# Performance work log

Measured on AMD Instinct MI355X. Metric: run time of the kernel, lower is better.

## Reference

```python
import jax, jax.numpy as jnp
import numpy as np

# module hyperparameters (match init_kwargs)
IN_PLANES = 64
OUT = 64            # out_planes
N_HASHES = 4
CHUNK = 25          # chunk_size
GROUPS = 8
KS = 56             # kernel_size == attended axis length H
GP = OUT // GROUPS  # group_planes = 8
EPS_N = 5e-5        # F.normalize eps
BN_EPS = 1e-5
F_GW, F_GV1, F_GV2 = 0.1, 0.1, 1.0


def l2norm(x, axis):
    # torch F.normalize(p=2, eps=EPS_N)
    n = jnp.sqrt(jnp.sum(x * x, axis=axis, keepdims=True))
    return x / jnp.maximum(n, EPS_N)


def setup_inputs() -> dict:
    key = jax.random.key(0)
    k1, k2, k3, k4 = jax.random.split(key, 4)
    x = jax.random.normal(k1, (2, IN_PLANES, KS, 56), jnp.float32)
    conv_w = jax.random.normal(k2, (OUT * 3 // 2, IN_PLANES), jnp.float32) * np.float32(np.sqrt(1.0 / IN_PLANES))
    bn_gamma = jnp.ones((OUT * 3 // 2,), jnp.float32)
    bn_beta = jnp.zeros((OUT * 3 // 2,), jnp.float32)
    relative = jax.random.normal(k3, (KS, GP * 3 // 2), jnp.float32) * np.float32(np.sqrt(1.0 / GP))
    # LSH random rotations: hash_buckets = min(56//25 + (56//25)%2, 10) = 2 -> hb//2 = 1
    rotations = jax.random.normal(k4, (OUT // 2, N_HASHES, 1), jnp.float32)
    return dict(x=x, conv_w=conv_w, bn_gamma=bn_gamma, bn_beta=bn_beta,
                relative=relative, rotations=rotations)


def reference(x, conv_w, bn_gamma, bn_beta, relative, rotations):
    # width=False: (N,C,H,W) -> (N,W,C,H), flatten batch with W
    N, C, Hax, W = x.shape
    x = jnp.transpose(x, (0, 3, 1, 2)).reshape(N * W, C, Hax)
    B, H = N * W, Hax
    hash_buckets = min(H // CHUNK + (H // CHUNK) % 2, 10)

    # 1x1 conv + eval-mode BatchNorm (running_mean=0, running_var=1)
    qkv = jnp.einsum('oc,bch->boh', conv_w, x)
    qkv = qkv / np.float32(np.sqrt(1.0 + BN_EPS)) * bn_gamma[None, :, None] + bn_beta[None, :, None]
    # NOTE: original uses raw reshape (B,C3,H) -> (B,H,C3), NOT a transpose
    qkv = qkv.reshape(B, H, OUT * 3 // 2)
    w_match = qkv[..., :OUT // 2]   # (B,H,out/2)
    v_match = qkv[..., OUT // 2:]   # (B,H,out)
    w_emb = relative[:, :GP // 2]
    v_emb = relative[:, GP // 2:]

    # LSH hashing (rotations shared across batch)
    rot = jnp.einsum('btf,fhi->bhti', w_match, rotations)
    rot = jnp.concatenate([rot, -rot], axis=-1)           # (B,nh,H,hash_buckets)
    codes = jnp.argmax(rot, axis=-1)
    codes = codes + (jnp.arange(N_HASHES) * hash_buckets)[None, :, None]
    codes = codes.reshape(B, N_HASHES * H)

    indices = jnp.argsort(codes, axis=-1)                 # stable sort into buckets
    undo = jnp.argsort(indices, axis=-1)
    mod = indices % H
    w_s = jnp.take_along_axis(w_match, mod[:, :, None], axis=1)
    v_s = jnp.take_along_axis(v_match, mod[:, :, None], axis=1)

    padding = (CHUNK - H % CHUNK) % CHUNK                 # 19 here
    w_b = w_s.reshape(B, N_HASHES, H, OUT // 2)
    v_b = v_s.reshape(B, N_HASHES, H, OUT)
    if padding:
        w_b = jnp.concatenate([w_b, w_b[:, :, -padding:, :]], axis=2)
        v_b = jnp.concatenate([v_b, v_b[:, :, -padding:, :]], axis=2)
        w_emb = jnp.concatenate([w_emb, w_emb[-padding:, :]], axis=0)
        v_emb = jnp.concatenate([v_emb, v_emb[-padding:, :]], axis=0)
    # raw reshapes, exactly as torch does (groups folded via flat reshape)
    w_b = w_b.reshape(B, GROUPS, N_HASHES, -1, CHUNK, GP // 2)
    v_b = v_b.reshape(B, GROUPS, N_HASHES, -1, CHUNK, GP)
    w_emb = w_emb.reshape(-1, CHUNK, GP // 2)             # (K,25,4)
    v_emb = v_emb.reshape(-1, CHUNK, GP)                  # (K,25,8)
    K = w_emb.shape[0]

    def adj(t):  # look-around over the chunk axis (dim 3), cat on dim 4
        return jnp.concatenate([t, jnp.roll(t, 1, axis=3), jnp.roll(t, -1, axis=3)], axis=4)

    def adj_emb(t):
        return jnp.concatenate([t, jnp.roll(t, 1, axis=0), jnp.roll(t, -1, axis=0)], axis=1)

    w_m = adj(l2norm(w_b, -1))
    v_a = adj(v_b)
    w_e = adj_emb(w_emb)
    v_e = adj_emb(v_emb)

    raw = jnp.einsum('bghkie,bghkje->bghkij', w_b, w_m)            # (B,g,h,K,25,75)
    emb_sc = F_GW * jnp.einsum('bghkie,kje->bghkij', w_b, w_e)
    ss = jnp.concatenate([raw, emb_sc], axis=1)                    # (B,2g,h,K,25,75)
    ss = l2norm(ss, 1).reshape(B, 2, GROUPS, N_HASHES, K, CHUNK, CHUNK * 3).sum(axis=1)

    bs = jax.nn.logsumexp(ss, axis=-1, keepdims=True)
    score = jnp.exp(ss - bs)
    bs = bs.reshape(B, GROUPS, N_HASHES, K * CHUNK)

    r_out = F_GV2 * jnp.einsum('bgukij,bgukje->bgukie', score, v_a)
    r_emb = F_GV1 * jnp.einsum('bgukij,kje->bgukie', score, v_e)
    ret = jnp.concatenate([r_out, r_emb], axis=-1)                 # (B,g,h,K,25,2*gp)
    ret = ret.reshape(B, N_HASHES, K, CHUNK, OUT * 2)              # raw reshape
    ret = ret.reshape(B, OUT * 2, N_HASHES, K, CHUNK)              # raw reshape
    ret = l2norm(ret, 1).reshape(B, N_HASHES, K, CHUNK, OUT, 2).sum(axis=-1)
    bs = l2norm(bs, 1).sum(axis=1)                                 # (B,h,K*25)

    ret = ret.reshape(B, N_HASHES, K * CHUNK, OUT)
    if padding:
        ret = ret[:, :, :-padding, :]
        bs = bs[:, :, :-padding]
    ret = ret.reshape(B, N_HASHES * H, OUT)
    bs = bs.reshape(B, N_HASHES * H)

    ret = jnp.take_along_axis(ret, undo[:, :, None], axis=1)      # unsort
    bs = jnp.take_along_axis(bs, undo, axis=1)
    ret = ret.reshape(B, N_HASHES, H, OUT)
    bs = bs.reshape(B, N_HASHES, H, 1)

    probs = jax.nn.softmax(bs, axis=1)
    ret = jnp.sum(ret * probs, axis=1)                             # (B,H,out)
    ret = ret.reshape(N, W, H, OUT)
    return jnp.transpose(ret, (0, 3, 2, 1))                        # (N,out,H,W)
```

## Files before the change

kernel.cpp:

```cpp
#include <hip/hip_runtime.h>
#include <math.h>


#define EPSN 5e-5f
#define INV_EPSN 20000.0f
#define LOG2E 1.4426950408889634f
#define LN2   0.6931471805599453f

__device__ __forceinline__ float dot4(const float4 a, const float4 b) {
    return a.x * b.x + a.y * b.y + a.z * b.z + a.w * b.w;
}
__device__ __forceinline__ void fma4(float4& a, float s, const float4 v) {
    a.x += s * v.x; a.y += s * v.y; a.z += s * v.z; a.w += s * v.w;
}

__global__ __launch_bounds__(256) void k12_qkv_sort(
        const float* __restrict__ x, const float* __restrict__ cw,
        const float* __restrict__ gamma, const float* __restrict__ beta,
        const float* __restrict__ rot, float* __restrict__ qkv,
        int* __restrict__ idx_buf) {
    __shared__ float xsT[56 * 68];
    __shared__ float cws[96 * 64];
    __shared__ float wm[56 * 32];
    __shared__ float rl[128];
    __shared__ float gs[96], bt[96];
    __shared__ int code[224];
    __shared__ int srt[224];
    const int b = blockIdx.x, n = b / 56, w = b % 56, tid = threadIdx.x;
    const float* xb = x + n * 200704 + w;
    #pragma unroll 7
    for (int i = tid; i < 3584; i += 256) {
        int c = i / 56, h = i % 56;
        xsT[h * 68 + c] = xb[c * 3136 + h * 56];
    }
    #pragma unroll 8
    for (int i = tid; i < 6144; i += 256) cws[i] = cw[i];
    if (tid < 128) rl[tid] = rot[tid];
    if (tid < 96) { gs[tid] = gamma[tid]; bt[tid] = beta[tid]; }
    __syncthreads();
    const float inv_s = 1.0f / sqrtf(1.0f + 1.0e-5f);
    for (int tl = tid; tl < 1344; tl += 256) {
        int oq = tl / 56, h = tl % 56;
        int o0 = oq * 4;
        float s0 = 0.f, s1 = 0.f, s2 = 0.f, s3 = 0.f;
        #pragma unroll
        for (int cs = 0; cs < 16; ++cs) {
            float4 xv = *(const float4*)&xsT[h * 68 + cs * 4];
            float4 c0 = *(const float4*)&cws[(o0 + 0) * 64 + cs * 4];
            float4 c1 = *(const float4*)&cws[(o0 + 1) * 64 + cs * 4];
            float4 c2 = *(const float4*)&cws[(o0 + 2) * 64 + cs * 4];
            float4 c3 = *(const float4*)&cws[(o0 + 3) * 64 + cs * 4];
            s0 += dot4(xv, c0); s1 += dot4(xv, c1);
            s2 += dot4(xv, c2); s3 += dot4(xv, c3);
        }
        #pragma unroll
        for (int qq = 0; qq < 4; ++qq) {
            int o = o0 + qq;
            float sv = (qq == 0) ? s0 : (qq == 1) ? s1 : (qq == 2) ? s2 : s3;
            float val = sv * inv_s * gs[o] + bt[o];
            int j = o * 56 + h;
            qkv[b * 5376 + j] = val;
            int f = j % 96;
            if (f < 32) wm[(j / 96) * 32 + f] = val;
        }
    }
    __syncthreads();
    if (tid < 224) {
        int u = tid / 56, t = tid % 56;
        float s = 0.f;
        #pragma unroll 8
        for (int f = 0; f < 32; ++f) s += wm[t * 32 + f] * rl[f * 4 + u];
        code[tid] = ((s < 0.f) ? 1 : 0) + 2 * u;
    }
    __syncthreads();
    if (tid < 224) {
        int c = code[tid], r = 0;
        #pragma unroll 8
        for (int p = 0; p < 224; ++p) {
            int cp = code[p];
            r += (int)((cp < c) | ((cp == c) & (p < tid)));
        }
        srt[r] = tid;
    }
    __syncthreads();
    if (tid < 224) idx_buf[b * 224 + tid] = srt[tid];
}

__global__ __launch_bounds__(256) void k3_attn(
        const float* __restrict__ qkv, const int* __restrict__ idx_buf,
        const float* __restrict__ rel, float* __restrict__ Rb,
        float* __restrict__ bsb) {
    __shared__ __align__(16) float Wc[8][3][25][4];
    __shared__ __align__(16) float Vb[8][3][25][8];
    __shared__ __align__(16) float WbK[8][25][4];
    __shared__ float DIT[75][25];
    __shared__ int ibL[224];
    const int b = blockIdx.x, u = blockIdx.y, k = blockIdx.z;
    const int tid = threadIdx.x;
    const float* q = qkv + b * 5376;

    if (tid < 224) ibL[tid] = idx_buf[b * 224 + tid];
    __syncthreads();

    #pragma unroll 3
    for (int idx = tid; idx < 600; idx += 256) {
        int i = idx % 25, kk = (idx / 25) % 3, g = idx / 75;
        int p0 = 1200 * g + 300 * u + 100 * kk + 4 * i;
        int h = p0 / 2400, r = p0 % 2400, t = r >> 5, f = r & 31;
        int row = (t < 56) ? t : t - 19;
        int tt = ibL[h * 56 + row] % 56;
        float4 v = *(const float4*)&q[tt * 96 + f];
        if (kk == k) *(float4*)&WbK[g][i][0] = v;
        float ni = fminf(__builtin_amdgcn_rsqf(dot4(v, v)), INV_EPSN);
        v.x *= ni; v.y *= ni; v.z *= ni; v.w *= ni;
        *(float4*)&Wc[g][kk][i][0] = v;
    }
    #pragma unroll 5
    for (int idx = tid; idx < 1200; idx += 256) {
        int half = idx & 1, fr = idx >> 1;
        int i = fr % 25, kk = (fr / 25) % 3, g = fr / 75;
        int p0 = 2400 * g + 600 * u + 200 * kk + 8 * i + 4 * half;
        int h = p0 / 4800, r = p0 % 4800, t = r >> 6, f = r & 63;
        int row = (t < 56) ? t : t - 19;
        int tt = ibL[h * 56 + row] % 56;
        *(float4*)&Vb[g][kk][i][4 * half] = *(const float4*)&q[tt * 96 + 32 + f];
    }
    __syncthreads();

    if (tid < 250) {
        const int i = tid % 25, jg = tid / 25;
        float4 wb8[8];
        #pragma unroll
        for (int g = 0; g < 8; ++g) wb8[g] = *(const float4*)&WbK[g][i][0];
        #pragma unroll
        for (int it = 0; it < 8; ++it) {
            int j = jg * 8 + it;
            if (j < 75) {
                int ks = j / 25, jj = j % 25;
                int roww = (j < 56) ? j : j - 19;
                float4 we = *(const float4*)&rel[roww * 12];
                we.x *= 0.1f; we.y *= 0.1f; we.z *= 0.1f; we.w *= 0.1f;
                float s2 = 0.f;
                #pragma unroll
                for (int g = 0; g < 8; ++g) {
                    float4 wcn = *(const float4*)&Wc[g][ks][jj][0];
                    float raw = dot4(wb8[g], wcn);
                    float emb = dot4(wb8[g], we);
                    s2 += raw * raw + emb * emb;
                }
                DIT[j][i] = fminf(__builtin_amdgcn_rsqf(s2), INV_EPSN);
            }
        }
    }
    __syncthreads();

    #pragma unroll 3
    for (int idx = tid; idx < 600; idx += 256) {
        int i = idx % 25, kk = (idx / 25) % 3, g = idx / 75;
        int tw = kk * 25 + i;
        int roww = (tw < 56) ? tw : tw - 19;
        float4 we = *(const float4*)&rel[roww * 12];
        float4 v = *(const float4*)&Wc[g][kk][i][0];
        v.x += 0.1f * we.x; v.y += 0.1f * we.y;
        v.z += 0.1f * we.z; v.w += 0.1f * we.w;
        *(float4*)&Wc[g][kk][i][0] = v;
    }
    __syncthreads();

    if (tid < 200) {
        const int g = tid & 7, i = tid >> 3;
        const float4 wbr = *(const float4*)&WbK[g][i][0];
        float se = 0.f;
        float4 a0 = {0,0,0,0}, a1 = {0,0,0,0}, a2 = {0,0,0,0}, a3 = {0,0,0,0};
        #pragma unroll
        for (int ks = 0; ks < 3; ++ks) {
            #pragma unroll
            for (int jj = 0; jj < 25; ++jj) {
                const int jP = ks * 25 + jj;
                const int roww = (jP < 56) ? jP : jP - 19;
                float di = DIT[jP][i];
                float e = __builtin_amdgcn_exp2f(
                    dot4(wbr, *(const float4*)&Wc[g][ks][jj][0]) * di * LOG2E);
                se += e;
                const float4* vv = (const float4*)&Vb[g][ks][jj][0];
                fma4(a0, e, vv[0]); fma4(a1, e, vv[1]);
                float4 ve0 = *(const float4*)&rel[roww * 12 + 4];
                float4 ve1 = *(const float4*)&rel[roww * 12 + 8];
                fma4(a2, e, ve0); fma4(a3, e, ve1);
            }
        }
        bsb[b * 2400 + g * 300 + u * 75 + k * 25 + i] =
            __builtin_amdgcn_logf(se) * LN2;
        const float rinv = 1.0f / se;
        const float r2 = 0.1f * rinv;
        a0.x *= rinv; a0.y *= rinv; a0.z *= rinv; a0.w *= rinv;
        a1.x *= rinv; a1.y *= rinv; a1.z *= rinv; a1.w *= rinv;
        a2.x *= r2;   a2.y *= r2;   a2.z *= r2;   a2.w *= r2;
        a3.x *= r2;   a3.y *= r2;   a3.z *= r2;   a3.w *= r2;
        float* rp = Rb + b * 38400 + 4800 * g + 1200 * u + 400 * k + 16 * i;
        ((float4*)rp)[0] = a0;
        ((float4*)rp)[1] = a1;
        ((float4*)rp)[2] = a2;
        ((float4*)rp)[3] = a3;
    }
}

__global__ __launch_bounds__(256) void k45_post(
        const float* __restrict__ Rb, const float* __restrict__ bsb,
        const int* __restrict__ idx_buf, float* __restrict__ out) {
    __shared__ float D[300];
    __shared__ float bsn[300];
    __shared__ float retU[224][32];
    __shared__ float bsU[224];
    __shared__ int idxL[224];
    const int b = blockIdx.x, oh = blockIdx.y, tid = threadIdx.x;
    const int n = b / 56, w = b % 56, o0 = oh * 32;
    const float* R = Rb + b * 38400;
    if (tid < 224) idxL[tid] = idx_buf[b * 224 + tid];
    for (int r = tid; r < 300; r += 256) {
        float s = 0.f;
        #pragma unroll 16
        for (int c = 0; c < 128; ++c) { float v = R[c * 300 + r]; s += v * v; }
        D[r] = fminf(__builtin_amdgcn_rsqf(s), INV_EPSN);
    }
    for (int idx = tid; idx < 300; idx += 256) {
        int u = idx / 75, t = idx % 75;
        float s2 = 0.f, sum = 0.f;
        #pragma unroll
        for (int g = 0; g < 8; ++g) {
            float v = bsb[b * 2400 + g * 300 + u * 75 + t];
            s2 += v * v; sum += v;
        }
        bsn[idx] = sum / fmaxf(sqrtf(s2), EPSN);
    }
    __syncthreads();
    if (tid < 224) {
        int u3 = tid / 56, t = tid % 56;
        bsU[idxL[tid]] = bsn[u3 * 75 + t];
    }
    #pragma unroll 4
    for (int idx = tid; idx < 224 * 32; idx += 256) {
        int p = idx >> 5, oc = idx & 31;
        int o = o0 + oc;
        int u3 = p / 56, t = p % 56;
        int k3 = t / 25, i3 = t % 25;
        int q0 = 9600 * u3 + 3200 * k3 + 128 * i3 + 2 * o;
        float2 rv = *(const float2*)&R[q0];
        int r0 = q0 % 300;
        float val = rv.x * D[r0] + rv.y * D[r0 + 1];
        retU[idxL[p]][oc] = val;
    }
    __syncthreads();
    for (int idx = tid; idx < 56 * 32; idx += 256) {
        int h = idx >> 5, oc = idx & 31;
        int o = o0 + oc;
        float b0 = bsU[h], b1 = bsU[56 + h], b2 = bsU[112 + h], b3 = bsU[168 + h];
        float m = fmaxf(fmaxf(b0, b1), fmaxf(b2, b3));
        float e0 = __builtin_amdgcn_exp2f((b0 - m) * LOG2E);
        float e1 = __builtin_amdgcn_exp2f((b1 - m) * LOG2E);
        float e2 = __builtin_amdgcn_exp2f((b2 - m) * LOG2E);
        float e3 = __builtin_amdgcn_exp2f((b3 - m) * LOG2E);
        float ps = e0 + e1 + e2 + e3;
        float val = (retU[h][oc] * e0 + retU[56 + h][oc] * e1 +
                     retU[112 + h][oc] * e2 + retU[168 + h][oc] * e3) / ps;
        out[((n * 64 + o) * 56 + h) * 56 + w] = val;
    }
}

extern "C" void kernel_launch(void* const* d_in, const int* in_sizes, int n_in,
                              void* d_out, int out_size, void* d_ws, size_t ws_size,
                              hipStream_t stream) {
    (void)in_sizes; (void)n_in; (void)out_size; (void)ws_size;
    const float* x     = (const float*)d_in[0];
    const float* cw    = (const float*)d_in[1];
    const float* gamma = (const float*)d_in[2];
    const float* beta  = (const float*)d_in[3];
    const float* rel   = (const float*)d_in[4];
    const float* rot   = (const float*)d_in[5];
    float* ws  = (float*)d_ws;
    float* qkv = ws;
    float* bsb = ws + 602112;
    float* Rb  = ws + 870912;
    int*   idx = (int*)(ws + 5171712);

    k12_qkv_sort<<<112, 256, 0, stream>>>(x, cw, gamma, beta, rot, qkv, idx);
    k3_attn<<<dim3(112, 4, 3), 256, 0, stream>>>(qkv, idx, rel, Rb, bsb);
    k45_post<<<dim3(112, 2), 256, 0, stream>>>(Rb, bsb, idx, (float*)d_out);
}
```

Measured before the change: 154.5 us.

## Pre-transpose input in a separate kernel and widen post kernel to 512 threads

Adds a transpose kernel that rewrites x into a (n,h,w,c) layout in workspace, aliased onto the attention output buffer. The qkv/sort kernel can then load each column with coalesced float4 reads instead of strided scalar gathers. The post kernel moves to 512 threads so each of the 300 norm rows gets its own thread, which removes the second pass for the leftover rows. The cost is an extra launch and an extra round trip of x through global memory.

```diff
diff --git a/kernel.cpp b/kernel.cpp
--- a/kernel.cpp
+++ b/kernel.cpp
@@ -14,8 +14,27 @@
     a.x += s * v.x; a.y += s * v.y; a.z += s * v.z; a.w += s * v.w;
 }
 
+__global__ __launch_bounds__(256) void k0_xT(
+        const float* __restrict__ x, float* __restrict__ xT) {
+    __shared__ float T[64][57];
+    const int n = blockIdx.x, h = blockIdx.y, tid = threadIdx.x;
+    const float* xb = x + n * 200704 + h * 56;
+    #pragma unroll 7
+    for (int i = tid; i < 3584; i += 256) {
+        int c = i / 56, w = i % 56;
+        T[c][w] = xb[c * 3136 + w];
+    }
+    __syncthreads();
+    float* xo = xT + n * 200704 + h * 3584;
+    #pragma unroll 7
+    for (int i = tid; i < 3584; i += 256) {
+        int w = i / 64, c = i % 64;
+        xo[w * 64 + c] = T[c][w];
+    }
+}
+
 __global__ __launch_bounds__(256) void k12_qkv_sort(
-        const float* __restrict__ x, const float* __restrict__ cw,
+        const float* __restrict__ xT, const float* __restrict__ cw,
         const float* __restrict__ gamma, const float* __restrict__ beta,
         const float* __restrict__ rot, float* __restrict__ qkv,
         int* __restrict__ idx_buf) {
@@ -27,11 +46,12 @@
     __shared__ int code[224];
     __shared__ int srt[224];
     const int b = blockIdx.x, n = b / 56, w = b % 56, tid = threadIdx.x;
-    const float* xb = x + n * 200704 + w;
-    #pragma unroll 7
-    for (int i = tid; i < 3584; i += 256) {
-        int c = i / 56, h = i % 56;
-        xsT[h * 68 + c] = xb[c * 3136 + h * 56];
+    const float* xTb = xT + n * 200704 + w * 64;
+    #pragma unroll 4
+    for (int i = tid; i < 896; i += 256) {
+        int h = i / 16, cq = i % 16;
+        *(float4*)&xsT[h * 68 + cq * 4] =
+            *(const float4*)&xTb[h * 3584 + cq * 4];
     }
     #pragma unroll 8
     for (int i = tid; i < 6144; i += 256) cws[i] = cw[i];
@@ -205,7 +225,7 @@
     }
 }
 
-__global__ __launch_bounds__(256) void k45_post(
+__global__ __launch_bounds__(512) void k45_post(
         const float* __restrict__ Rb, const float* __restrict__ bsb,
         const int* __restrict__ idx_buf, float* __restrict__ out) {
     __shared__ float D[300];
@@ -217,21 +237,22 @@
     const int n = b / 56, w = b % 56, o0 = oh * 32;
     const float* R = Rb + b * 38400;
     if (tid < 224) idxL[tid] = idx_buf[b * 224 + tid];
-    for (int r = tid; r < 300; r += 256) {
+    if (tid < 300) {
         float s = 0.f;
         #pragma unroll 16
-        for (int c = 0; c < 128; ++c) { float v = R[c * 300 + r]; s += v * v; }
-        D[r] = fminf(__builtin_amdgcn_rsqf(s), INV_EPSN);
-    }
-    for (int idx = tid; idx < 300; idx += 256) {
-        int u = idx / 75, t = idx % 75;
+        for (int c = 0; c < 128; ++c) { float v = R[c * 300 + tid]; s += v * v; }
+        D[tid] = fminf(__builtin_amdgcn_rsqf(s), INV_EPSN);
+    }
+    if (tid >= 512 - 300 + 88) { }
+    if (tid < 300) {
+        int u = tid / 75, t = tid % 75;
         float s2 = 0.f, sum = 0.f;
         #pragma unroll
         for (int g = 0; g < 8; ++g) {
             float v = bsb[b * 2400 + g * 300 + u * 75 + t];
             s2 += v * v; sum += v;
         }
-        bsn[idx] = sum / fmaxf(sqrtf(s2), EPSN);
+        bsn[tid] = sum / fmaxf(sqrtf(s2), EPSN);
     }
     __syncthreads();
     if (tid < 224) {
@@ -239,7 +260,7 @@
         bsU[idxL[tid]] = bsn[u3 * 75 + t];
     }
     #pragma unroll 4
-    for (int idx = tid; idx < 224 * 32; idx += 256) {
+    for (int idx = tid; idx < 224 * 32; idx += 512) {
         int p = idx >> 5, oc = idx & 31;
         int o = o0 + oc;
         int u3 = p / 56, t = p % 56;
@@ -251,7 +272,7 @@
         retU[idxL[p]][oc] = val;
     }
     __syncthreads();
-    for (int idx = tid; idx < 56 * 32; idx += 256) {
+    for (int idx = tid; idx < 56 * 32; idx += 512) {
         int h = idx >> 5, oc = idx & 31;
         int o = o0 + oc;
         float b0 = bsU[h], b1 = bsU[56 + h], b2 = bsU[112 + h], b3 = bsU[168 + h];
@@ -281,9 +302,11 @@
     float* qkv = ws;
     float* bsb = ws + 602112;
     float* Rb  = ws + 870912;
+    float* xT  = Rb;
     int*   idx = (int*)(ws + 5171712);
 
-    k12_qkv_sort<<<112, 256, 0, stream>>>(x, cw, gamma, beta, rot, qkv, idx);
+    k0_xT<<<dim3(2, 56), 256, 0, stream>>>(x, xT);
+    k12_qkv_sort<<<112, 256, 0, stream>>>(xT, cw, gamma, beta, rot, qkv, idx);
     k3_attn<<<dim3(112, 4, 3), 256, 0, stream>>>(qkv, idx, rel, Rb, bsb);
-    k45_post<<<dim3(112, 2), 256, 0, stream>>>(Rb, bsb, idx, (float*)d_out);
-}
+    k45_post<<<dim3(112, 2), 512, 0, stream>>>(Rb, bsb, idx, (float*)d_out);
+}
```

Result: faster. 150.7 us (-2.4%).
